# Kernel tuning notes

Hardware: AMD Instinct MI355X
Metric: run time of the kernel (lower is better)

## Reference

```python
import jax, jax.numpy as jnp
import numpy as np

HEADS = 16
LN_EPS = 1e-5


def setup_inputs() -> dict:
    key = jax.random.key(0)
    ks = jax.random.split(key, 8)
    B, S, D = 2, 2048, 1024
    F = 4 * D
    std = 0.02
    return {
        "x": jax.random.normal(ks[0], (B, S, D), jnp.float32),
        # QKV projections (stored as (in, out)); kaiming-normal-like scale
        "Wq": jax.random.normal(ks[1], (D, D), jnp.float32) * std,
        "bq": jnp.zeros((D,), jnp.float32),
        "Wk": jax.random.normal(ks[2], (D, D), jnp.float32) * std,
        "bk": jnp.zeros((D,), jnp.float32),
        "Wv": jax.random.normal(ks[3], (D, D), jnp.float32) * std,
        "bv": jnp.zeros((D,), jnp.float32),
        # FFN
        "W1": jax.random.normal(ks[4], (D, F), jnp.float32) * std,
        "b1": jnp.zeros((F,), jnp.float32),
        "W2": jax.random.normal(ks[5], (F, D), jnp.float32) * std,
        "b2": jnp.zeros((D,), jnp.float32),
        # LayerNorm
        "gamma": jnp.ones((D,), jnp.float32),
        "beta": jnp.zeros((D,), jnp.float32),
    }


def reference(x, Wq, bq, Wk, bk, Wv, bv, W1, b1, W2, b2, gamma, beta):
    B, S, D = x.shape
    H = HEADS
    hd = D // H
    # QKV projections -> [B, H, S, hd]
    Q = (x @ Wq + bq).reshape(B, S, H, hd).transpose(0, 2, 1, 3)
    K = (x @ Wk + bk).reshape(B, S, H, hd).transpose(0, 2, 1, 3)
    V = (x @ Wv + bv).reshape(B, S, H, hd).transpose(0, 2, 1, 3)
    # scores scaled by sqrt(embedding_dim), faithful to source (not head_dim)
    scores = jnp.einsum('bhqd,bhkd->bhqk', Q, K) / jnp.sqrt(jnp.asarray(D, x.dtype))
    attn = jax.nn.softmax(scores, axis=-1)
    # diagonal_training: zero the diagonal of the post-softmax attention matrix
    attn = attn * (1.0 - jnp.eye(S, dtype=attn.dtype))
    out = jnp.einsum('bhqk,bhkd->bhqd', attn, V)
    out = out.transpose(0, 2, 1, 3).reshape(B, S, D)
    # dropout is identity in eval mode
    h = jax.nn.gelu(out @ W1 + b1, approximate=False) @ W2 + b2
    # LayerNorm
    mu = jnp.mean(h, axis=-1, keepdims=True)
    var = jnp.var(h, axis=-1, keepdims=True)
    return (h - mu) * jax.lax.rsqrt(var + LN_EPS) * gamma + beta
```

## Files before the change

### kernel.cpp

```cpp
#include <hip/hip_runtime.h>

using bf16x8 = __attribute__((ext_vector_type(8))) short;
using f32x4  = __attribute__((ext_vector_type(4))) float;

__device__ __forceinline__ float b2f(ushort u) {
  union { unsigned int i; float f; } v; v.i = ((unsigned int)u) << 16; return v.f;
}
__device__ __forceinline__ ushort f2b(float f) {
  unsigned int x = __float_as_uint(f);
  unsigned int r = (x + 0x7FFFu + ((x >> 16) & 1u)) >> 16;
  return (ushort)r;
}
__device__ __forceinline__ unsigned cvt_pk_bf16(float a, float b) {
  unsigned r;
  asm("v_cvt_pk_bf16_f32 %0, %1, %2" : "=v"(r) : "v"(a), "v"(b));
  return r;
}

__device__ __forceinline__ void gld_lds16(const void* g, void* l) {
  __builtin_amdgcn_global_load_lds(
      (const __attribute__((address_space(1))) void*)g,
      (__attribute__((address_space(3))) void*)l, 16, 0, 0);
}


__global__ void cast_bf16_kernel(const float* __restrict__ in, ushort* __restrict__ out, int n) {
  int i = (blockIdx.x * blockDim.x + threadIdx.x) * 4;
  if (i < n) {
    float4 v = *(const float4*)(in + i);
    ushort4 o = make_ushort4(f2b(v.x), f2b(v.y), f2b(v.z), f2b(v.w));
    *(ushort4*)(out + i) = o;
  }
}

__global__ void transpose_cast_kernel(const float* __restrict__ in, ushort* __restrict__ out,
                                      int R, int C) {
  __shared__ float tile[32][33];
  int tx = threadIdx.x, ty = threadIdx.y;
  int cb = blockIdx.x * 32, rb = blockIdx.y * 32;
  for (int i = ty; i < 32; i += 8)
    tile[i][tx] = in[(size_t)(rb + i) * C + (cb + tx)];
  __syncthreads();
  for (int i = ty; i < 32; i += 8)
    out[(size_t)(cb + i) * R + (rb + tx)] = f2b(tile[tx][i]);
}

__global__ void transpose_v_kernel(const ushort* __restrict__ V, ushort* __restrict__ Vt) {
  __shared__ ushort t[32][33];
  int bh = blockIdx.z;
  int b = bh >> 4, h = bh & 15;
  int s0 = blockIdx.x * 32, d0 = blockIdx.y * 32;
  const ushort* Vbp = V + ((size_t)b * 2048) * 1024 + h * 64;
  ushort* Vtb = Vt + (size_t)bh * 64 * 2048;
  int tx = threadIdx.x, ty = threadIdx.y;
  for (int i = ty; i < 32; i += 8) t[i][tx] = Vbp[(size_t)(s0 + i) * 1024 + d0 + tx];
  __syncthreads();
  for (int i = ty; i < 32; i += 8) Vtb[(size_t)(d0 + i) * 2048 + s0 + tx] = t[tx][i];
}


template<int EPI>
__global__ __launch_bounds__(512) void gemm256(
    const ushort* __restrict__ A, const ushort* __restrict__ Bt,
    const float* __restrict__ bias, void* __restrict__ Cout,
    int M, int N, int K)
{
  extern __shared__ ushort lds[];

  const int nwg = gridDim.x * gridDim.y;
  const int bid = blockIdx.y * gridDim.x + blockIdx.x;
  const int cpx = nwg >> 3;
  const int swz = (bid & 7) * cpx + (bid >> 3);
  const int bm = (swz % gridDim.x) * 256;
  const int bn = (swz / gridDim.x) * 256;

  const int tid = threadIdx.x;
  const int lane = tid & 63, w = tid >> 6;
  const int wr = w >> 2, wc = w & 3;
  const int g = lane >> 4, c = lane & 15;
  const int swz8 = ((g ^ ((c >> 1) & 3)) * 8);

  const int srow = tid >> 2;
  const int scol = (((tid & 3) ^ ((srow >> 1) & 3)) * 8);
  const ushort* gA = A  + (size_t)(bm + srow) * K + scol;
  const ushort* gB = Bt + (size_t)(bn + srow) * K + scol;
  const size_t rowK128 = (size_t)128 * K;

  const int NT = K / 32;
  f32x4 acc[8][4] = {};

  #pragma unroll
  for (int kt = 0; kt < 2; ++kt) {
    ushort* sA = &lds[kt * 16384];
    gld_lds16(gA + (size_t)kt * 32,            sA + tid * 8);
    gld_lds16(gA + rowK128 + (size_t)kt * 32,  sA + 4096 + tid * 8);
    gld_lds16(gB + (size_t)kt * 32,            sA + 8192 + tid * 8);
    gld_lds16(gB + rowK128 + (size_t)kt * 32,  sA + 8192 + 4096 + tid * 8);
  }

  for (int kt = 0; kt < NT; ++kt) {
    ushort* sA = &lds[(kt % 3) * 16384];
    ushort* sB = sA + 8192;
    const int stage_kt = kt + 2;
    ushort* sS = &lds[(stage_kt % 3) * 16384];

    __builtin_amdgcn_sched_barrier(0);
    if (kt + 1 < NT) asm volatile("s_waitcnt vmcnt(4)" ::: "memory");
    else             asm volatile("s_waitcnt vmcnt(0)" ::: "memory");
    __builtin_amdgcn_s_barrier();
    __builtin_amdgcn_sched_barrier(0);

    bf16x8 bf[4], af[4];
    #pragma unroll
    for (int n = 0; n < 4; ++n)
      bf[n] = *(const bf16x8*)&sB[(wc * 64 + n * 16 + c) * 32 + swz8];
    #pragma unroll
    for (int m = 0; m < 4; ++m)
      af[m] = *(const bf16x8*)&sA[(wr * 128 + m * 16 + c) * 32 + swz8];
    if (stage_kt < NT) {
      gld_lds16(gA + (size_t)stage_kt * 32,           sS + tid * 8);
      gld_lds16(gA + rowK128 + (size_t)stage_kt * 32, sS + 4096 + tid * 8);
    }
    asm volatile("s_waitcnt lgkmcnt(0)" ::: "memory");
    __builtin_amdgcn_sched_barrier(0);
    __builtin_amdgcn_s_setprio(1);
    #pragma unroll
    for (int m = 0; m < 4; ++m)
      #pragma unroll
      for (int n = 0; n < 4; ++n)
        acc[m][n] = __builtin_amdgcn_mfma_f32_16x16x32_bf16(af[m], bf[n], acc[m][n], 0, 0, 0);
    __builtin_amdgcn_s_setprio(0);
    __builtin_amdgcn_sched_barrier(0);

    #pragma unroll
    for (int m = 0; m < 4; ++m)
      af[m] = *(const bf16x8*)&sA[(wr * 128 + 64 + m * 16 + c) * 32 + swz8];
    if (stage_kt < NT) {
      gld_lds16(gB + (size_t)stage_kt * 32,           sS + 8192 + tid * 8);
      gld_lds16(gB + rowK128 + (size_t)stage_kt * 32, sS + 8192 + 4096 + tid * 8);
    }
    asm volatile("s_waitcnt lgkmcnt(0)" ::: "memory");
    __builtin_amdgcn_sched_barrier(0);
    __builtin_amdgcn_s_setprio(1);
    #pragma unroll
    for (int m = 0; m < 4; ++m)
      #pragma unroll
      for (int n = 0; n < 4; ++n)
        acc[4 + m][n] = __builtin_amdgcn_mfma_f32_16x16x32_bf16(af[m], bf[n], acc[4 + m][n], 0, 0, 0);
    __builtin_amdgcn_s_setprio(0);
    __builtin_amdgcn_sched_barrier(0);
  }

  __syncthreads();
  ushort* eb = &lds[w * 1088];
  const int er = lane >> 3;
  const int es = (lane & 7) * 8;
  float bia[4];
  #pragma unroll
  for (int n = 0; n < 4; ++n) bia[n] = bias[bn + wc * 64 + n * 16 + c];

  #pragma unroll
  for (int mf = 0; mf < 8; ++mf) {
    #pragma unroll
    for (int n = 0; n < 4; ++n) {
      #pragma unroll
      for (int r = 0; r < 4; ++r) {
        float v = acc[mf][n][r] + bia[n];
        if (EPI == 1) {
          float u = 0.7978845608028654f * (v + 0.044715f * v * v * v);
          float au = fabsf(u);
          float e = __expf(-2.0f * au);
          float th = (1.0f - e) / (1.0f + e);
          th = copysignf(th, u);
          v = 0.5f * v * (1.0f + th);
        }
        eb[(g * 4 + r) * 68 + n * 16 + c] = f2b(v);
      }
    }
    asm volatile("" ::: "memory");
    bf16x8 v0 = *(const bf16x8*)&eb[er * 68 + es];
    bf16x8 v1 = *(const bf16x8*)&eb[(er + 8) * 68 + es];
    int grow = bm + wr * 128 + mf * 16 + er;
    int gcol = bn + wc * 64 + es;
    if (EPI == 3) {
      ushort* dst = (ushort*)Cout + (size_t)(gcol >> 10) * 4194304 + (gcol & 1023);
      *(bf16x8*)(dst + (size_t)grow * 1024) = v0;
      *(bf16x8*)(dst + (size_t)(grow + 8) * 1024) = v1;
    } else {
      ushort* dst = (ushort*)Cout + gcol;
      *(bf16x8*)(dst + (size_t)grow * N) = v0;
      *(bf16x8*)(dst + (size_t)(grow + 8) * N) = v1;
    }
    asm volatile("" ::: "memory");
  }
}


#define BM 128
#define BN 128
#define BK 32

__global__ __launch_bounds__(256) void gemm_bf16_f32(
    const ushort* __restrict__ A, const ushort* __restrict__ Bt,
    float* __restrict__ C0, float* __restrict__ C1,
    float* __restrict__ C2, float* __restrict__ C3,
    int M, int N, int Kstride, int k_len)
{
  __shared__ ushort Asm_[2][BM * BK];
  __shared__ ushort Bsm_[2][BN * BK];
  const int bm = blockIdx.x * BM, bn = blockIdx.y * BN;
  const int k_begin = blockIdx.z * k_len;
  const int tid = threadIdx.x;
  const int lane = tid & 63, w = tid >> 6;
  const int wm = (w >> 1) * 64, wn = (w & 1) * 64;
  const int g = lane >> 4, c = lane & 15;
  const int swz8 = ((g ^ ((c >> 1) & 3)) * 8);
  const int srow = tid >> 2;
  const int scol = (((tid & 3) ^ ((srow >> 1) & 3)) * 8);
  const int soff = srow * 32 + (tid & 3) * 8;

  const ushort* gA0 = A  + (size_t)(bm + srow) * Kstride + k_begin + scol;
  const ushort* gA1 = gA0 + (size_t)64 * Kstride;
  const ushort* gB0 = Bt + (size_t)(bn + srow) * Kstride + k_begin + scol;
  const ushort* gB1 = gB0 + (size_t)64 * Kstride;

  f32x4 acc[4][4] = {};
  const int nt = k_len / BK;

  gld_lds16(gA0, &Asm_[0][soff]);
  gld_lds16(gA1, &Asm_[0][64 * 32 + soff]);
  gld_lds16(gB0, &Bsm_[0][soff]);
  gld_lds16(gB1, &Bsm_[0][64 * 32 + soff]);
  __syncthreads();

  int cur = 0;
  for (int t = 0; t < nt; ++t) {
    if (t + 1 < nt) {
      int k0 = (t + 1) * BK;
      gld_lds16(gA0 + k0, &Asm_[cur ^ 1][soff]);
      gld_lds16(gA1 + k0, &Asm_[cur ^ 1][64 * 32 + soff]);
      gld_lds16(gB0 + k0, &Bsm_[cur ^ 1][soff]);
      gld_lds16(gB1 + k0, &Bsm_[cur ^ 1][64 * 32 + soff]);
    }
    bf16x8 af[4], bfr[4];
    #pragma unroll
    for (int m = 0; m < 4; ++m)
      af[m] = *(const bf16x8*)&Asm_[cur][(wm + m * 16 + c) * 32 + swz8];
    #pragma unroll
    for (int n = 0; n < 4; ++n)
      bfr[n] = *(const bf16x8*)&Bsm_[cur][(wn + n * 16 + c) * 32 + swz8];
    #pragma unroll
    for (int m = 0; m < 4; ++m)
      #pragma unroll
      for (int n = 0; n < 4; ++n)
        acc[m][n] = __builtin_amdgcn_mfma_f32_16x16x32_bf16(af[m], bfr[n], acc[m][n], 0, 0, 0);
    __syncthreads();
    cur ^= 1;
  }

  float* dst = C0;
  if (blockIdx.z == 1) dst = C1;
  else if (blockIdx.z == 2) dst = C2;
  else if (blockIdx.z == 3) dst = C3;

  #pragma unroll
  for (int n = 0; n < 4; ++n) {
    int col = bn + wn + n * 16 + c;
    #pragma unroll
    for (int m = 0; m < 4; ++m)
      #pragma unroll
      for (int r = 0; r < 4; ++r) {
        int row = bm + wm + m * 16 + g * 4 + r;
        dst[(size_t)row * N + col] = acc[m][n][r];
      }
  }
}


#define ATT_SC2 0.0450842202f

__global__ __launch_bounds__(512) void attn_kernel(
    const ushort* __restrict__ Q, const ushort* __restrict__ K,
    const ushort* __restrict__ V, const ushort* __restrict__ Vt,
    ushort* __restrict__ Out)
{
  const int bh = blockIdx.y;
  const int b = bh >> 4, h = bh & 15;
  const int q0 = blockIdx.x * 128;
  const int tid = threadIdx.x;
  const int w = tid >> 6, lane = tid & 63;
  const int hi = lane >> 4, c = lane & 15;
  const int qw = q0 + w * 16;

  const size_t boff = ((size_t)b * 2048) * 1024 + h * 64;
  const ushort* Qp = Q + boff;
  const ushort* Kp = K + boff;
  const ushort* Vp = V + boff;
  const ushort* Vtb = Vt + (size_t)bh * 64 * 2048;

  __shared__ ushort Ksm[2][64 * 64];
  __shared__ ushort Vsm[2][64 * 64];
  __shared__ ushort Psm[8][16 * 72];

  const int srow = tid >> 3;
  const int sslot = tid & 7;
  const int scolx = ((sslot ^ (srow & 7)) * 8);
  const ushort* gK = Kp + (size_t)srow * 1024 + scolx;
  const ushort* gV = Vtb + (size_t)srow * 2048 + scolx;

  bf16x8 qf0 = *(const bf16x8*)(Qp + (size_t)(qw + c) * 1024 + hi * 8);
  bf16x8 qf1 = *(const bf16x8*)(Qp + (size_t)(qw + c) * 1024 + 32 + hi * 8);

  f32x4 acc[4] = {};
  float m_run = -1e30f, l_run = 0.f;

  gld_lds16(gK, &Ksm[0][tid * 8]);
  gld_lds16(gV, &Vsm[0][tid * 8]);
  __syncthreads();

  const int nt = 2048 / 64;
  for (int t = 0; t < nt; ++t) {
    const int buf = t & 1;
    if (t + 1 < nt) {
      gld_lds16(gK + (size_t)(t + 1) * 64 * 1024, &Ksm[buf ^ 1][tid * 8]);
      gld_lds16(gV + (size_t)(t + 1) * 64,        &Vsm[buf ^ 1][tid * 8]);
    }

    f32x4 sv[4];
    #pragma unroll
    for (int sub = 0; sub < 4; ++sub) {
      int rr = sub * 16 + c;
      int sw = (rr & 7) * 8;
      bf16x8 k0 = *(const bf16x8*)&Ksm[buf][rr * 64 + ((hi * 8) ^ sw)];
      bf16x8 k1 = *(const bf16x8*)&Ksm[buf][rr * 64 + ((32 + hi * 8) ^ sw)];
      f32x4 z = {};
      __builtin_amdgcn_s_setprio(1);
      z = __builtin_amdgcn_mfma_f32_16x16x32_bf16(k0, qf0, z, 0, 0, 0);
      z = __builtin_amdgcn_mfma_f32_16x16x32_bf16(k1, qf1, z, 0, 0, 0);
      __builtin_amdgcn_s_setprio(0);
      #pragma unroll
      for (int r = 0; r < 4; ++r) sv[sub][r] = z[r] * ATT_SC2;
    }

    float tm = -1e30f;
    #pragma unroll
    for (int sub = 0; sub < 4; ++sub)
      #pragma unroll
      for (int r = 0; r < 4; ++r) tm = fmaxf(tm, sv[sub][r]);
    tm = fmaxf(tm, __shfl_xor(tm, 16));
    tm = fmaxf(tm, __shfl_xor(tm, 32));
    float mnew = fmaxf(m_run, tm);
    float p[16];
    float psum = 0.f;
    #pragma unroll
    for (int sub = 0; sub < 4; ++sub)
      #pragma unroll
      for (int r = 0; r < 4; ++r) { float e = exp2f(sv[sub][r] - mnew); p[sub * 4 + r] = e; psum += e; }
    psum += __shfl_xor(psum, 16);
    psum += __shfl_xor(psum, 32);
    float f = exp2f(m_run - mnew);
    l_run = l_run * f + psum;
    m_run = mnew;

    #pragma unroll
    for (int r = 0; r < 4; ++r) {
      float fr = __shfl(f, hi * 4 + r, 16);
      #pragma unroll
      for (int dsub = 0; dsub < 4; ++dsub) acc[dsub][r] *= fr;
    }

    #pragma unroll
    for (int sub = 0; sub < 4; ++sub) {
      uint2 pk;
      pk.x = cvt_pk_bf16(p[sub * 4 + 0], p[sub * 4 + 1]);
      pk.y = cvt_pk_bf16(p[sub * 4 + 2], p[sub * 4 + 3]);
      *(uint2*)&Psm[w][c * 72 + sub * 16 + hi * 4] = pk;
    }
    asm volatile("" ::: "memory");

    bf16x8 pa0 = *(const bf16x8*)&Psm[w][c * 72 + hi * 8];
    bf16x8 pa1 = *(const bf16x8*)&Psm[w][c * 72 + 32 + hi * 8];
    __builtin_amdgcn_s_setprio(1);
    #pragma unroll
    for (int dsub = 0; dsub < 4; ++dsub) {
      int rr = dsub * 16 + c;
      int sw = (rr & 7) * 8;
      bf16x8 v0 = *(const bf16x8*)&Vsm[buf][rr * 64 + ((hi * 8) ^ sw)];
      bf16x8 v1 = *(const bf16x8*)&Vsm[buf][rr * 64 + ((32 + hi * 8) ^ sw)];
      acc[dsub] = __builtin_amdgcn_mfma_f32_16x16x32_bf16(pa0, v0, acc[dsub], 0, 0, 0);
      acc[dsub] = __builtin_amdgcn_mfma_f32_16x16x32_bf16(pa1, v1, acc[dsub], 0, 0, 0);
    }
    __builtin_amdgcn_s_setprio(0);

    __syncthreads();
  }

  #pragma unroll
  for (int r = 0; r < 4; ++r) {
    int q = qw + hi * 4 + r;
    float part = 0.f;
    #pragma unroll
    for (int t = 0; t < 4; ++t)
      part += b2f(Qp[(size_t)q * 1024 + c * 4 + t]) * b2f(Kp[(size_t)q * 1024 + c * 4 + t]);
    #pragma unroll
    for (int off = 1; off < 16; off <<= 1) part += __shfl_xor(part, off);
    float mq = __shfl(m_run, hi * 4 + r, 16);
    float lq = __shfl(l_run, hi * 4 + r, 16);
    float pqq = exp2f(part * ATT_SC2 - mq);
    float inv = 1.f / lq;
    #pragma unroll
    for (int dsub = 0; dsub < 4; ++dsub) {
      float vq = b2f(Vp[(size_t)q * 1024 + dsub * 16 + c]);
      float o = (acc[dsub][r] - pqq * vq) * inv;
      Out[((size_t)(b * 2048 + q) * 16 + h) * 64 + dsub * 16 + c] = f2b(o);
    }
  }
}


__global__ __launch_bounds__(256) void ln_kernel(float* __restrict__ h,
                                                 const float* __restrict__ p1,
                                                 const float* __restrict__ p2,
                                                 const float* __restrict__ p3,
                                                 const float* __restrict__ b2,
                                                 const float* __restrict__ gamma,
                                                 const float* __restrict__ beta, int np) {
  int row = blockIdx.x, tid = threadIdx.x;
  float* hr = h + (size_t)row * 1024;
  float4 v = ((const float4*)hr)[tid];
  float4 p = ((const float4*)(p1 + (size_t)row * 1024))[tid];
  float4 bb = ((const float4*)b2)[tid];
  v.x += p.x + bb.x; v.y += p.y + bb.y; v.z += p.z + bb.z; v.w += p.w + bb.w;
  if (np == 4) {
    float4 a = ((const float4*)(p2 + (size_t)row * 1024))[tid];
    float4 d = ((const float4*)(p3 + (size_t)row * 1024))[tid];
    v.x += a.x + d.x; v.y += a.y + d.y; v.z += a.z + d.z; v.w += a.w + d.w;
  }
  float s = v.x + v.y + v.z + v.w;
  #pragma unroll
  for (int off = 1; off < 64; off <<= 1) s += __shfl_xor(s, off);
  __shared__ float red[2][4];
  int wv = tid >> 6, lane = tid & 63;
  if (lane == 0) red[0][wv] = s;
  __syncthreads();
  float mu = (red[0][0] + red[0][1] + red[0][2] + red[0][3]) * (1.0f / 1024.0f);
  float dx = v.x - mu, dy = v.y - mu, dz = v.z - mu, dw = v.w - mu;
  float q = dx * dx + dy * dy + dz * dz + dw * dw;
  #pragma unroll
  for (int off = 1; off < 64; off <<= 1) q += __shfl_xor(q, off);
  if (lane == 0) red[1][wv] = q;
  __syncthreads();
  float var = (red[1][0] + red[1][1] + red[1][2] + red[1][3]) * (1.0f / 1024.0f);
  float is = rsqrtf(var + 1e-5f);
  float4 gm = ((const float4*)gamma)[tid];
  float4 bt = ((const float4*)beta)[tid];
  float4 o;
  o.x = dx * is * gm.x + bt.x;
  o.y = dy * is * gm.y + bt.y;
  o.z = dz * is * gm.z + bt.z;
  o.w = dw * is * gm.w + bt.w;
  ((float4*)hr)[tid] = o;
}


extern "C" void kernel_launch(void* const* d_in, const int* in_sizes, int n_in,
                              void* d_out, int out_size, void* d_ws, size_t ws_size,
                              hipStream_t stream) {
  const float* x  = (const float*)d_in[0];
  const float* Wq = (const float*)d_in[1];
  const float* bq = (const float*)d_in[2];
  const float* Wk = (const float*)d_in[3];
  const float* bk = (const float*)d_in[4];
  const float* Wv = (const float*)d_in[5];
  const float* bv = (const float*)d_in[6];
  const float* W1 = (const float*)d_in[7];
  const float* b1 = (const float*)d_in[8];
  const float* W2 = (const float*)d_in[9];
  const float* b2 = (const float*)d_in[10];
  const float* gamma = (const float*)d_in[11];
  const float* beta  = (const float*)d_in[12];
  float* out = (float*)d_out;

  char* ws = (char*)d_ws;
  const size_t MB = 1u << 20;
  ushort* xb    = (ushort*)(ws + 0);
  ushort* Wqkvt = (ushort*)(ws + 8 * MB);
  ushort* Qb    = (ushort*)(ws + 14 * MB);
  ushort* Kb    = (ushort*)(ws + 22 * MB);
  ushort* Vb    = (ushort*)(ws + 30 * MB);
  ushort* Vt    = (ushort*)(ws + 38 * MB);
  ushort* AO    = (ushort*)(ws + 46 * MB);
  ushort* W1t   = (ushort*)(ws + 54 * MB);
  ushort* h1    = (ushort*)(ws + 0);
  ushort* W2t   = (ushort*)(ws + 32 * MB);
  float*  p1    = (float*)(ws + 40 * MB);
  float*  p2    = (float*)(ws + 56 * MB);
  float*  p3    = (float*)(ws + 72 * MB);
  float*  bqkv  = (float*)(ws + 46 * MB);

  const bool split4 = (ws_size >= (size_t)89 * MB);

  (void)hipMemcpyAsync(bqkv,        bq, 4096, hipMemcpyDeviceToDevice, stream);
  (void)hipMemcpyAsync(bqkv + 1024, bk, 4096, hipMemcpyDeviceToDevice, stream);
  (void)hipMemcpyAsync(bqkv + 2048, bv, 4096, hipMemcpyDeviceToDevice, stream);

  dim3 tb(32, 8);
  cast_bf16_kernel<<<4096, 256, 0, stream>>>(x, xb, 4194304);
  transpose_cast_kernel<<<dim3(32, 32), tb, 0, stream>>>(Wq, Wqkvt, 1024, 1024);
  transpose_cast_kernel<<<dim3(32, 32), tb, 0, stream>>>(Wk, Wqkvt + 1024 * 1024, 1024, 1024);
  transpose_cast_kernel<<<dim3(32, 32), tb, 0, stream>>>(Wv, Wqkvt + 2 * 1024 * 1024, 1024, 1024);
  transpose_cast_kernel<<<dim3(128, 32), tb, 0, stream>>>(W1, W1t, 1024, 4096);

  gemm256<3><<<dim3(16, 12), 512, 98304, stream>>>(xb, Wqkvt, bqkv, Qb, 4096, 3072, 1024);

  transpose_v_kernel<<<dim3(64, 2, 32), tb, 0, stream>>>(Vb, Vt);

  attn_kernel<<<dim3(16, 32), 512, 0, stream>>>(Qb, Kb, Vb, Vt, AO);

  transpose_cast_kernel<<<dim3(32, 128), tb, 0, stream>>>(W2, W2t, 4096, 1024);

  gemm256<1><<<dim3(16, 16), 512, 98304, stream>>>(AO, W1t, b1, h1, 4096, 4096, 1024);

  if (split4) {
    gemm_bf16_f32<<<dim3(32, 8, 4), 256, 0, stream>>>(h1, W2t, out, p1, p2, p3,
                                                      4096, 1024, 4096, 1024);
    ln_kernel<<<4096, 256, 0, stream>>>(out, p1, p2, p3, b2, gamma, beta, 4);
  } else {
    gemm_bf16_f32<<<dim3(32, 8, 2), 256, 0, stream>>>(h1, W2t, out, p1, nullptr, nullptr,
                                                      4096, 1024, 4096, 2048);
    ln_kernel<<<4096, 256, 0, stream>>>(out, p1, nullptr, nullptr, b2, gamma, beta, 2);
  }
}
```

Measured before the change: 253.1 us.

## Rework GEMM to K64 double-buffered tiles and streamline attention softmax

The 256x256 GEMM drops its hand-scheduled triple-buffered K=32 pipeline for a simpler double-buffered K=64 loop with 128KB LDS and an XOR swizzle, issuing 32 MFMAs per k-substep. The attention kernel moves to a 1D grid with a tile swizzle for L2 locality, folds the score scale into Q once, and skips the running-max rescale unless the max grows by more than a threshold (lazy rescaling). The GEMM change gives up the careful waitcnt-based overlap, and the larger LDS footprint may lower occupancy. Pre-scaling Q in bf16 adds rounding error.

```diff
diff --git a/kernel.cpp b/kernel.cpp
--- a/kernel.cpp
+++ b/kernel.cpp
@@ -77,82 +77,62 @@
   const int tid = threadIdx.x;
   const int lane = tid & 63, w = tid >> 6;
   const int wr = w >> 2, wc = w & 3;
-  const int g = lane >> 4, c = lane & 15;
-  const int swz8 = ((g ^ ((c >> 1) & 3)) * 8);
-
-  const int srow = tid >> 2;
-  const int scol = (((tid & 3) ^ ((srow >> 1) & 3)) * 8);
-  const ushort* gA = A  + (size_t)(bm + srow) * K + scol;
-  const ushort* gB = Bt + (size_t)(bn + srow) * K + scol;
-  const size_t rowK128 = (size_t)128 * K;
-
-  const int NT = K / 32;
+  const int hi = lane >> 4, c = lane & 15;
+
+  const int srow0 = tid >> 3;
+  const int scolx = (((tid & 7) ^ (srow0 & 7)) * 8);
+  const ushort* gA = A  + (size_t)(bm + srow0) * K + scolx;
+  const ushort* gB = Bt + (size_t)(bn + srow0) * K + scolx;
+
+  const int NT = K / 64;
   f32x4 acc[8][4] = {};
 
-  #pragma unroll
-  for (int kt = 0; kt < 2; ++kt) {
-    ushort* sA = &lds[kt * 16384];
-    gld_lds16(gA + (size_t)kt * 32,            sA + tid * 8);
-    gld_lds16(gA + rowK128 + (size_t)kt * 32,  sA + 4096 + tid * 8);
-    gld_lds16(gB + (size_t)kt * 32,            sA + 8192 + tid * 8);
-    gld_lds16(gB + rowK128 + (size_t)kt * 32,  sA + 8192 + 4096 + tid * 8);
-  }
-
-  for (int kt = 0; kt < NT; ++kt) {
-    ushort* sA = &lds[(kt % 3) * 16384];
-    ushort* sB = sA + 8192;
-    const int stage_kt = kt + 2;
-    ushort* sS = &lds[(stage_kt % 3) * 16384];
-
-    __builtin_amdgcn_sched_barrier(0);
-    if (kt + 1 < NT) asm volatile("s_waitcnt vmcnt(4)" ::: "memory");
-    else             asm volatile("s_waitcnt vmcnt(0)" ::: "memory");
-    __builtin_amdgcn_s_barrier();
-    __builtin_amdgcn_sched_barrier(0);
-
-    bf16x8 bf[4], af[4];
-    #pragma unroll
-    for (int n = 0; n < 4; ++n)
-      bf[n] = *(const bf16x8*)&sB[(wc * 64 + n * 16 + c) * 32 + swz8];
-    #pragma unroll
-    for (int m = 0; m < 4; ++m)
-      af[m] = *(const bf16x8*)&sA[(wr * 128 + m * 16 + c) * 32 + swz8];
-    if (stage_kt < NT) {
-      gld_lds16(gA + (size_t)stage_kt * 32,           sS + tid * 8);
-      gld_lds16(gA + rowK128 + (size_t)stage_kt * 32, sS + 4096 + tid * 8);
-    }
-    asm volatile("s_waitcnt lgkmcnt(0)" ::: "memory");
-    __builtin_amdgcn_sched_barrier(0);
-    __builtin_amdgcn_s_setprio(1);
-    #pragma unroll
-    for (int m = 0; m < 4; ++m)
-      #pragma unroll
-      for (int n = 0; n < 4; ++n)
-        acc[m][n] = __builtin_amdgcn_mfma_f32_16x16x32_bf16(af[m], bf[n], acc[m][n], 0, 0, 0);
-    __builtin_amdgcn_s_setprio(0);
-    __builtin_amdgcn_sched_barrier(0);
-
-    #pragma unroll
-    for (int m = 0; m < 4; ++m)
-      af[m] = *(const bf16x8*)&sA[(wr * 128 + 64 + m * 16 + c) * 32 + swz8];
-    if (stage_kt < NT) {
-      gld_lds16(gB + (size_t)stage_kt * 32,           sS + 8192 + tid * 8);
-      gld_lds16(gB + rowK128 + (size_t)stage_kt * 32, sS + 8192 + 4096 + tid * 8);
-    }
-    asm volatile("s_waitcnt lgkmcnt(0)" ::: "memory");
-    __builtin_amdgcn_sched_barrier(0);
-    __builtin_amdgcn_s_setprio(1);
-    #pragma unroll
-    for (int m = 0; m < 4; ++m)
-      #pragma unroll
-      for (int n = 0; n < 4; ++n)
-        acc[4 + m][n] = __builtin_amdgcn_mfma_f32_16x16x32_bf16(af[m], bf[n], acc[4 + m][n], 0, 0, 0);
-    __builtin_amdgcn_s_setprio(0);
-    __builtin_amdgcn_sched_barrier(0);
-  }
-
-  __syncthreads();
+  auto STAGE = [&](int buf, int t) {
+    ushort* bA = lds + buf * 32768;
+    ushort* bB = bA + 16384;
+    const size_t ko = (size_t)t * 64;
+    #pragma unroll
+    for (int ch = 0; ch < 4; ++ch) {
+      gld_lds16(gA + (size_t)ch * 64 * K + ko, bA + ch * 4096 + tid * 8);
+      gld_lds16(gB + (size_t)ch * 64 * K + ko, bB + ch * 4096 + tid * 8);
+    }
+  };
+
+  STAGE(0, 0);
+  __syncthreads();
+
+  int cur = 0;
+  for (int t = 0; t < NT; ++t) {
+    if (t + 1 < NT) STAGE(cur ^ 1, t + 1);
+    const ushort* sA = lds + cur * 32768;
+    const ushort* sB = sA + 16384;
+    #pragma unroll
+    for (int kk = 0; kk < 2; ++kk) {
+      bf16x8 bf[4], af[8];
+      #pragma unroll
+      for (int n = 0; n < 4; ++n) {
+        int row = wc * 64 + n * 16 + c;
+        bf[n] = *(const bf16x8*)&sB[row * 64 + (((kk * 4 + hi) ^ (c & 7)) * 8)];
+      }
+      #pragma unroll
+      for (int m = 0; m < 8; ++m) {
+        int row = wr * 128 + m * 16 + c;
+        af[m] = *(const bf16x8*)&sA[row * 64 + (((kk * 4 + hi) ^ (c & 7)) * 8)];
+      }
+      __builtin_amdgcn_s_setprio(1);
+      #pragma unroll
+      for (int m = 0; m < 8; ++m)
+        #pragma unroll
+        for (int n = 0; n < 4; ++n)
+          acc[m][n] = __builtin_amdgcn_mfma_f32_16x16x32_bf16(af[m], bf[n], acc[m][n], 0, 0, 0);
+      __builtin_amdgcn_s_setprio(0);
+    }
+    __syncthreads();
+    cur ^= 1;
+  }
+
   ushort* eb = &lds[w * 1088];
+  const int g = hi;
   const int er = lane >> 3;
   const int es = (lane & 7) * 8;
   float bia[4];
@@ -284,9 +264,11 @@
     const ushort* __restrict__ V, const ushort* __restrict__ Vt,
     ushort* __restrict__ Out)
 {
-  const int bh = blockIdx.y;
+  const int bid = blockIdx.x;
+  const int tile = (bid & 7) * 64 + (bid >> 3);
+  const int bh = tile >> 4;
+  const int q0 = (tile & 15) * 128;
   const int b = bh >> 4, h = bh & 15;
-  const int q0 = blockIdx.x * 128;
   const int tid = threadIdx.x;
   const int w = tid >> 6, lane = tid & 63;
   const int hi = lane >> 4, c = lane & 15;
@@ -310,6 +292,15 @@
 
   bf16x8 qf0 = *(const bf16x8*)(Qp + (size_t)(qw + c) * 1024 + hi * 8);
   bf16x8 qf1 = *(const bf16x8*)(Qp + (size_t)(qw + c) * 1024 + 32 + hi * 8);
+  {
+    ushort* q0p = (ushort*)&qf0;
+    ushort* q1p = (ushort*)&qf1;
+    #pragma unroll
+    for (int j = 0; j < 8; ++j) {
+      q0p[j] = f2b(b2f(q0p[j]) * ATT_SC2);
+      q1p[j] = f2b(b2f(q1p[j]) * ATT_SC2);
+    }
+  }
 
   f32x4 acc[4] = {};
   float m_run = -1e30f, l_run = 0.f;
@@ -327,6 +318,7 @@
     }
 
     f32x4 sv[4];
+    __builtin_amdgcn_s_setprio(1);
     #pragma unroll
     for (int sub = 0; sub < 4; ++sub) {
       int rr = sub * 16 + c;
@@ -334,13 +326,11 @@
       bf16x8 k0 = *(const bf16x8*)&Ksm[buf][rr * 64 + ((hi * 8) ^ sw)];
       bf16x8 k1 = *(const bf16x8*)&Ksm[buf][rr * 64 + ((32 + hi * 8) ^ sw)];
       f32x4 z = {};
-      __builtin_amdgcn_s_setprio(1);
       z = __builtin_amdgcn_mfma_f32_16x16x32_bf16(k0, qf0, z, 0, 0, 0);
       z = __builtin_amdgcn_mfma_f32_16x16x32_bf16(k1, qf1, z, 0, 0, 0);
-      __builtin_amdgcn_s_setprio(0);
-      #pragma unroll
-      for (int r = 0; r < 4; ++r) sv[sub][r] = z[r] * ATT_SC2;
-    }
+      sv[sub] = z;
+    }
+    __builtin_amdgcn_s_setprio(0);
 
     float tm = -1e30f;
     #pragma unroll
@@ -349,25 +339,29 @@
       for (int r = 0; r < 4; ++r) tm = fmaxf(tm, sv[sub][r]);
     tm = fmaxf(tm, __shfl_xor(tm, 16));
     tm = fmaxf(tm, __shfl_xor(tm, 32));
-    float mnew = fmaxf(m_run, tm);
+
+    if (!__all(tm <= m_run + 8.0f)) {
+      float mnew = fmaxf(m_run, tm);
+      float f = exp2f(m_run - mnew);
+      l_run *= f;
+      #pragma unroll
+      for (int r = 0; r < 4; ++r) {
+        float fr = __shfl(f, hi * 4 + r, 16);
+        #pragma unroll
+        for (int dsub = 0; dsub < 4; ++dsub) acc[dsub][r] *= fr;
+      }
+      m_run = mnew;
+    }
+
     float p[16];
     float psum = 0.f;
     #pragma unroll
     for (int sub = 0; sub < 4; ++sub)
       #pragma unroll
-      for (int r = 0; r < 4; ++r) { float e = exp2f(sv[sub][r] - mnew); p[sub * 4 + r] = e; psum += e; }
+      for (int r = 0; r < 4; ++r) { float e = exp2f(sv[sub][r] - m_run); p[sub * 4 + r] = e; psum += e; }
     psum += __shfl_xor(psum, 16);
     psum += __shfl_xor(psum, 32);
-    float f = exp2f(m_run - mnew);
-    l_run = l_run * f + psum;
-    m_run = mnew;
-
-    #pragma unroll
-    for (int r = 0; r < 4; ++r) {
-      float fr = __shfl(f, hi * 4 + r, 16);
-      #pragma unroll
-      for (int dsub = 0; dsub < 4; ++dsub) acc[dsub][r] *= fr;
-    }
+    l_run += psum;
 
     #pragma unroll
     for (int sub = 0; sub < 4; ++sub) {
@@ -511,15 +505,15 @@
   transpose_cast_kernel<<<dim3(32, 32), tb, 0, stream>>>(Wv, Wqkvt + 2 * 1024 * 1024, 1024, 1024);
   transpose_cast_kernel<<<dim3(128, 32), tb, 0, stream>>>(W1, W1t, 1024, 4096);
 
-  gemm256<3><<<dim3(16, 12), 512, 98304, stream>>>(xb, Wqkvt, bqkv, Qb, 4096, 3072, 1024);
+  gemm256<3><<<dim3(16, 12), 512, 131072, stream>>>(xb, Wqkvt, bqkv, Qb, 4096, 3072, 1024);
 
   transpose_v_kernel<<<dim3(64, 2, 32), tb, 0, stream>>>(Vb, Vt);
 
-  attn_kernel<<<dim3(16, 32), 512, 0, stream>>>(Qb, Kb, Vb, Vt, AO);
+  attn_kernel<<<512, 512, 0, stream>>>(Qb, Kb, Vb, Vt, AO);
 
   transpose_cast_kernel<<<dim3(32, 128), tb, 0, stream>>>(W2, W2t, 4096, 1024);
 
-  gemm256<1><<<dim3(16, 16), 512, 98304, stream>>>(AO, W1t, b1, h1, 4096, 4096, 1024);
+  gemm256<1><<<dim3(16, 16), 512, 131072, stream>>>(AO, W1t, b1, h1, 4096, 4096, 1024);
 
   if (split4) {
     gemm_bf16_f32<<<dim3(32, 8, 4), 256, 0, stream>>>(h1, W2t, out, p1, p2, p3,
```

Result: faster. 247.0 us (-2.4%).
